# Performance work log

Measured on AMD Instinct MI355X. Metric: run time of the kernel, lower is better.

Reference implementation:

```python
import jax, jax.numpy as jnp
import numpy as np

N, D = 65536, 512

def setup_inputs() -> dict:
    key = jax.random.key(0)
    k1, k2, k3, k4, k5 = jax.random.split(key, 5)
    lim = 1.0 / np.sqrt(D)
    inputs = jax.random.normal(k1, (N, D), dtype=jnp.float32)
    key_w = jax.random.uniform(k2, (1, D), minval=-lim, maxval=lim, dtype=jnp.float32)
    key_b = jax.random.uniform(k3, (1,), minval=-lim, maxval=lim, dtype=jnp.float32)
    value_w = jax.random.uniform(k4, (D, D), minval=-lim, maxval=lim, dtype=jnp.float32)
    value_b = jax.random.uniform(k5, (D,), minval=-lim, maxval=lim, dtype=jnp.float32)
    return {"inputs": inputs, "key_w": key_w, "key_b": key_b,
            "value_w": value_w, "value_b": value_b}

def reference(inputs, key_w, key_b, value_w, value_b):
    # key: [N,1], value: [N,D] (torch Linear: x @ W.T + b)
    k = inputs @ key_w.T + key_b            # [N,1]
    v = inputs @ value_w.T + value_b        # [N,D]
    # Reassociate (v @ inputs.T) @ k == v @ (inputs.T @ k): avoids O(N^2) intermediate
    s = inputs.T @ k                        # [D,1]
    x = v @ s                               # [N,1]
    return jax.nn.softmax(x, axis=0)        # softmax over nodes (dim=0)
```

## Files before the change

kernel.cpp:

```cpp
#include <hip/hip_runtime.h>
#include <float.h>

#define NROWS 65536
#define DDIM  512

#define WS_T   4096
#define WS_MP  4608
#define WS_LP  5632

__global__ __launch_bounds__(256, 3) void kA(const float* __restrict__ in,
                                             const float* __restrict__ key_w,
                                             const float* __restrict__ key_b,
                                             float* __restrict__ s8) {
    const int tid  = threadIdx.x;
    const int lane = tid & 63;
    const int wv   = tid >> 6;
    const int q    = lane >> 4;
    const int u    = lane & 15;
    const int gw   = blockIdx.x * 4 + wv;

    const float4* kw4 = (const float4*)key_w;
    float4 kw[8];
    #pragma unroll
    for (int j = 0; j < 8; ++j) kw[j] = kw4[u + j * 16];
    const float kb = key_b[0];

    float4 acc[8];
    #pragma unroll
    for (int j = 0; j < 8; ++j) acc[j] = make_float4(0.f, 0.f, 0.f, 0.f);

    const int rowbase = gw * 16;
    #pragma unroll
    for (int it = 0; it < 4; ++it) {
        const int row = rowbase + it * 4 + q;
        const float4* r4 = (const float4*)(in + (size_t)row * DDIM);
        float4 v[8];
        #pragma unroll
        for (int j = 0; j < 8; ++j) v[j] = r4[u + j * 16];
        float p = 0.f;
        #pragma unroll
        for (int j = 0; j < 8; ++j)
            p += v[j].x * kw[j].x + v[j].y * kw[j].y
               + v[j].z * kw[j].z + v[j].w * kw[j].w;
        #pragma unroll
        for (int o = 1; o < 16; o <<= 1) p += __shfl_xor(p, o, 64);
        const float k = p + kb;
        #pragma unroll
        for (int j = 0; j < 8; ++j) {
            acc[j].x += k * v[j].x; acc[j].y += k * v[j].y;
            acc[j].z += k * v[j].z; acc[j].w += k * v[j].w;
        }
    }

    #pragma unroll
    for (int o = 16; o < 64; o <<= 1) {
        #pragma unroll
        for (int j = 0; j < 8; ++j) {
            acc[j].x += __shfl_xor(acc[j].x, o, 64);
            acc[j].y += __shfl_xor(acc[j].y, o, 64);
            acc[j].z += __shfl_xor(acc[j].z, o, 64);
            acc[j].w += __shfl_xor(acc[j].w, o, 64);
        }
    }

    __shared__ float sb[4][DDIM];
    if (q == 0) {
        #pragma unroll
        for (int j = 0; j < 8; ++j) {
            const int c = u * 4 + j * 64;
            sb[wv][c]     = acc[j].x;
            sb[wv][c + 1] = acc[j].y;
            sb[wv][c + 2] = acc[j].z;
            sb[wv][c + 3] = acc[j].w;
        }
    }
    __syncthreads();

    float* dst = s8 + (size_t)(blockIdx.x & 7) * DDIM;
    atomicAdd(&dst[tid],       sb[0][tid]     + sb[1][tid]     + sb[2][tid]     + sb[3][tid]);
    atomicAdd(&dst[tid + 256], sb[0][tid+256] + sb[1][tid+256] + sb[2][tid+256] + sb[3][tid+256]);
}

__global__ __launch_bounds__(512) void kB(const float* __restrict__ vw,
                                          const float* __restrict__ s8,
                                          float* __restrict__ t) {
    const int j = threadIdx.x;
    float acc = 0.f;
    #pragma unroll
    for (int ii = 0; ii < 8; ++ii) {
        const int i = blockIdx.x * 8 + ii;
        float si = 0.f;
        #pragma unroll
        for (int c = 0; c < 8; ++c) si += s8[c * 512 + i];
        acc += vw[(size_t)i * 512 + j] * si;
    }
    atomicAdd(&t[j], acc);
}

__global__ __launch_bounds__(256, 4) void kC(const float* __restrict__ in,
                                             const float* __restrict__ t,
                                             float* __restrict__ x,
                                             float* __restrict__ mpart,
                                             float* __restrict__ lpart) {
    const int tid  = threadIdx.x;
    const int lane = tid & 63;
    const int wv   = tid >> 6;
    const int q    = lane >> 4;
    const int u    = lane & 15;
    const int gw   = blockIdx.x * 4 + wv;

    const float4* t4 = (const float4*)t;
    float4 tt[8];
    #pragma unroll
    for (int j = 0; j < 8; ++j) tt[j] = t4[u + j * 16];

    float m = -FLT_MAX, l = 0.f;
    const int rowbase = gw * 16;
    #pragma unroll
    for (int it = 0; it < 4; ++it) {
        const int row = rowbase + it * 4 + q;
        const float4* r4 = (const float4*)(in + (size_t)row * DDIM);
        float4 v[8];
        #pragma unroll
        for (int j = 0; j < 8; ++j) v[j] = r4[u + j * 16];
        float p = 0.f;
        #pragma unroll
        for (int j = 0; j < 8; ++j)
            p += v[j].x * tt[j].x + v[j].y * tt[j].y
               + v[j].z * tt[j].z + v[j].w * tt[j].w;
        #pragma unroll
        for (int o = 1; o < 16; o <<= 1) p += __shfl_xor(p, o, 64);
        if (u == 0) x[row] = p;
        const float mn = fmaxf(m, p);
        l = l * __expf(m - mn) + __expf(p - mn);
        m = mn;
    }

    #pragma unroll
    for (int o = 16; o < 64; o <<= 1) {
        const float mo = __shfl_xor(m, o, 64);
        const float lo = __shfl_xor(l, o, 64);
        const float mn = fmaxf(m, mo);
        l = l * __expf(m - mn) + lo * __expf(mo - mn);
        m = mn;
    }
    __shared__ float ms[4], ls[4];
    if (lane == 0) { ms[wv] = m; ls[wv] = l; }
    __syncthreads();
    if (tid == 0) {
        m = ms[0]; l = ls[0];
        #pragma unroll
        for (int w = 1; w < 4; ++w) {
            const float mn = fmaxf(m, ms[w]);
            l = l * __expf(m - mn) + ls[w] * __expf(ms[w] - mn);
            m = mn;
        }
        mpart[blockIdx.x] = m;
        lpart[blockIdx.x] = l;
    }
}

__global__ __launch_bounds__(256) void kE(float* __restrict__ x,
                                          const float* __restrict__ mpart,
                                          const float* __restrict__ lpart) {
    const int tid  = threadIdx.x;
    const int lane = tid & 63;
    const int wv   = tid >> 6;

    float m = -FLT_MAX, l = 0.f;
    #pragma unroll
    for (int j = 0; j < 4; ++j) {
        const float mp = mpart[tid * 4 + j];
        const float lp = lpart[tid * 4 + j];
        const float mn = fmaxf(m, mp);
        l = l * __expf(m - mn) + lp * __expf(mp - mn);
        m = mn;
    }
    #pragma unroll
    for (int o = 1; o < 64; o <<= 1) {
        const float mo = __shfl_xor(m, o, 64);
        const float lo = __shfl_xor(l, o, 64);
        const float mn = fmaxf(m, mo);
        l = l * __expf(m - mn) + lo * __expf(mo - mn);
        m = mn;
    }
    __shared__ float ms[4], ls[4];
    __shared__ float Ms, Ls;
    if (lane == 0) { ms[wv] = m; ls[wv] = l; }
    __syncthreads();
    if (tid == 0) {
        m = ms[0]; l = ls[0];
        #pragma unroll
        for (int w = 1; w < 4; ++w) {
            const float mn = fmaxf(m, ms[w]);
            l = l * __expf(m - mn) + ls[w] * __expf(ms[w] - mn);
            m = mn;
        }
        Ms = m; Ls = l;
    }
    __syncthreads();

    float4* x4 = (float4*)x;
    const int i = blockIdx.x * 256 + tid;
    float4 v = x4[i];
    const float inv = 1.0f / Ls;
    v.x = __expf(v.x - Ms) * inv;
    v.y = __expf(v.y - Ms) * inv;
    v.z = __expf(v.z - Ms) * inv;
    v.w = __expf(v.w - Ms) * inv;
    x4[i] = v;
}

extern "C" void kernel_launch(void* const* d_in, const int* in_sizes, int n_in,
                              void* d_out, int out_size, void* d_ws, size_t ws_size,
                              hipStream_t stream) {
    const float* in    = (const float*)d_in[0];
    const float* key_w = (const float*)d_in[1];
    const float* key_b = (const float*)d_in[2];
    const float* vw    = (const float*)d_in[3];

    float* ws    = (float*)d_ws;
    float* s8    = ws;
    float* t     = ws + WS_T;
    float* mpart = ws + WS_MP;
    float* lpart = ws + WS_LP;
    float* out   = (float*)d_out;

    kA<<<1024, 256, 0, stream>>>(in, key_w, key_b, s8);
    kB<<<64, 512, 0, stream>>>(vw, s8, t);
    kC<<<1024, 256, 0, stream>>>(in, t, out, mpart, lpart);
    kE<<<64, 256, 0, stream>>>(out, mpart, lpart);
}
```

Baseline: 220.5 us.

## Map one row per wavefront in key and score kernels to cut registers

Kernels kA and kC now have a whole 64-lane wavefront handle each row, with every lane loading two float4s, instead of splitting four rows across 16-lane groups with eight float4s each. This removes the per-lane arrays of 8 float4s, which lowers register pressure. kA goes to 8 rows per wave over twice as many blocks, and its launch bound rises to 4 blocks per CU. The cost is a full 64-lane shuffle reduction per row and fewer independent loads in flight per lane, which may hurt latency hiding on a memory-bound pass. kA also issues twice as many atomics into s8.

```diff
diff --git a/kernel.cpp b/kernel.cpp
--- a/kernel.cpp
+++ b/kernel.cpp
@@ -8,72 +8,42 @@
 #define WS_MP  4608
 #define WS_LP  5632
 
-__global__ __launch_bounds__(256, 3) void kA(const float* __restrict__ in,
+__global__ __launch_bounds__(256, 4) void kA(const float* __restrict__ in,
                                              const float* __restrict__ key_w,
                                              const float* __restrict__ key_b,
                                              float* __restrict__ s8) {
     const int tid  = threadIdx.x;
     const int lane = tid & 63;
     const int wv   = tid >> 6;
-    const int q    = lane >> 4;
-    const int u    = lane & 15;
     const int gw   = blockIdx.x * 4 + wv;
 
     const float4* kw4 = (const float4*)key_w;
-    float4 kw[8];
+    const float4 kw0 = kw4[lane];
+    const float4 kw1 = kw4[64 + lane];
+    const float  kb  = key_b[0];
+
+    float4 a0 = make_float4(0.f, 0.f, 0.f, 0.f);
+    float4 a1 = make_float4(0.f, 0.f, 0.f, 0.f);
+
+    const int rowbase = gw * 8;
     #pragma unroll
-    for (int j = 0; j < 8; ++j) kw[j] = kw4[u + j * 16];
-    const float kb = key_b[0];
-
-    float4 acc[8];
-    #pragma unroll
-    for (int j = 0; j < 8; ++j) acc[j] = make_float4(0.f, 0.f, 0.f, 0.f);
-
-    const int rowbase = gw * 16;
-    #pragma unroll
-    for (int it = 0; it < 4; ++it) {
-        const int row = rowbase + it * 4 + q;
-        const float4* r4 = (const float4*)(in + (size_t)row * DDIM);
-        float4 v[8];
+    for (int r = 0; r < 8; ++r) {
+        const float4* r4 = (const float4*)(in + (size_t)(rowbase + r) * DDIM);
+        const float4 v0 = r4[lane];
+        const float4 v1 = r4[64 + lane];
+        float p = v0.x*kw0.x + v0.y*kw0.y + v0.z*kw0.z + v0.w*kw0.w
+                + v1.x*kw1.x + v1.y*kw1.y + v1.z*kw1.z + v1.w*kw1.w;
         #pragma unroll
-        for (int j = 0; j < 8; ++j) v[j] = r4[u + j * 16];
-        float p = 0.f;
-        #pragma unroll
-        for (int j = 0; j < 8; ++j)
-            p += v[j].x * kw[j].x + v[j].y * kw[j].y
-               + v[j].z * kw[j].z + v[j].w * kw[j].w;
-        #pragma unroll
-        for (int o = 1; o < 16; o <<= 1) p += __shfl_xor(p, o, 64);
+        for (int o = 1; o < 64; o <<= 1) p += __shfl_xor(p, o, 64);
         const float k = p + kb;
-        #pragma unroll
-        for (int j = 0; j < 8; ++j) {
-            acc[j].x += k * v[j].x; acc[j].y += k * v[j].y;
-            acc[j].z += k * v[j].z; acc[j].w += k * v[j].w;
-        }
-    }
-
-    #pragma unroll
-    for (int o = 16; o < 64; o <<= 1) {
-        #pragma unroll
-        for (int j = 0; j < 8; ++j) {
-            acc[j].x += __shfl_xor(acc[j].x, o, 64);
-            acc[j].y += __shfl_xor(acc[j].y, o, 64);
-            acc[j].z += __shfl_xor(acc[j].z, o, 64);
-            acc[j].w += __shfl_xor(acc[j].w, o, 64);
-        }
+        a0.x += k*v0.x; a0.y += k*v0.y; a0.z += k*v0.z; a0.w += k*v0.w;
+        a1.x += k*v1.x; a1.y += k*v1.y; a1.z += k*v1.z; a1.w += k*v1.w;
     }
 
     __shared__ float sb[4][DDIM];
-    if (q == 0) {
-        #pragma unroll
-        for (int j = 0; j < 8; ++j) {
-            const int c = u * 4 + j * 64;
-            sb[wv][c]     = acc[j].x;
-            sb[wv][c + 1] = acc[j].y;
-            sb[wv][c + 2] = acc[j].z;
-            sb[wv][c + 3] = acc[j].w;
-        }
-    }
+    float4* srow = (float4*)sb[wv];
+    srow[lane]      = a0;
+    srow[64 + lane] = a1;
     __syncthreads();
 
     float* dst = s8 + (size_t)(blockIdx.x & 7) * DDIM;
@@ -105,45 +75,29 @@
     const int tid  = threadIdx.x;
     const int lane = tid & 63;
     const int wv   = tid >> 6;
-    const int q    = lane >> 4;
-    const int u    = lane & 15;
     const int gw   = blockIdx.x * 4 + wv;
 
     const float4* t4 = (const float4*)t;
-    float4 tt[8];
-    #pragma unroll
-    for (int j = 0; j < 8; ++j) tt[j] = t4[u + j * 16];
+    const float4 t0 = t4[lane];
+    const float4 t1 = t4[64 + lane];
 
     float m = -FLT_MAX, l = 0.f;
     const int rowbase = gw * 16;
     #pragma unroll
-    for (int it = 0; it < 4; ++it) {
-        const int row = rowbase + it * 4 + q;
-        const float4* r4 = (const float4*)(in + (size_t)row * DDIM);
-        float4 v[8];
+    for (int r = 0; r < 16; ++r) {
+        const float4* r4 = (const float4*)(in + (size_t)(rowbase + r) * DDIM);
+        const float4 v0 = r4[lane];
+        const float4 v1 = r4[64 + lane];
+        float p = v0.x*t0.x + v0.y*t0.y + v0.z*t0.z + v0.w*t0.w
+                + v1.x*t1.x + v1.y*t1.y + v1.z*t1.z + v1.w*t1.w;
         #pragma unroll
-        for (int j = 0; j < 8; ++j) v[j] = r4[u + j * 16];
-        float p = 0.f;
-        #pragma unroll
-        for (int j = 0; j < 8; ++j)
-            p += v[j].x * tt[j].x + v[j].y * tt[j].y
-               + v[j].z * tt[j].z + v[j].w * tt[j].w;
-        #pragma unroll
-        for (int o = 1; o < 16; o <<= 1) p += __shfl_xor(p, o, 64);
-        if (u == 0) x[row] = p;
+        for (int o = 1; o < 64; o <<= 1) p += __shfl_xor(p, o, 64);
+        if (lane == 0) x[rowbase + r] = p;
         const float mn = fmaxf(m, p);
         l = l * __expf(m - mn) + __expf(p - mn);
         m = mn;
     }
 
-    #pragma unroll
-    for (int o = 16; o < 64; o <<= 1) {
-        const float mo = __shfl_xor(m, o, 64);
-        const float lo = __shfl_xor(l, o, 64);
-        const float mn = fmaxf(m, mo);
-        l = l * __expf(m - mn) + lo * __expf(mo - mn);
-        m = mn;
-    }
     __shared__ float ms[4], ls[4];
     if (lane == 0) { ms[wv] = m; ls[wv] = l; }
     __syncthreads();
@@ -226,7 +180,7 @@
     float* lpart = ws + WS_LP;
     float* out   = (float*)d_out;
 
-    kA<<<1024, 256, 0, stream>>>(in, key_w, key_b, s8);
+    kA<<<2048, 256, 0, stream>>>(in, key_w, key_b, s8);
     kB<<<64, 512, 0, stream>>>(vw, s8, t);
     kC<<<1024, 256, 0, stream>>>(in, t, out, mpart, lpart);
     kE<<<64, 256, 0, stream>>>(out, mpart, lpart);
```

New measurement: 222.1 us. Within noise of the previous version (+0.7%).
